# Optimization experiments

Measured on AMD Instinct MI355X. Metric: run time of the kernel, lower is better.

Reference implementation:

```python
import jax, jax.numpy as jnp
import numpy as np

N_TIME, N_BATCH, N_STATE, N_FORCE = 64, 8192, 32, 16
DT = 0.05          # implicit (backward-Euler) step size
NEWTON_ITERS = 6   # fixed Newton-Raphson iteration count (converges well below fp32 eps here)


def setup_inputs() -> dict:
    key = jax.random.key(0)
    k = jax.random.split(key, 5)
    return {
        "y0": jax.random.normal(k[0], (N_BATCH, N_STATE), jnp.float32) * 0.1,
        "forces": jax.random.normal(k[1], (N_TIME, N_BATCH, N_FORCE), jnp.float32),
        "W": jax.random.normal(k[2], (N_STATE, N_STATE), jnp.float32) / np.float32(np.sqrt(N_STATE)),
        "U": jax.random.normal(k[3], (N_STATE, N_FORCE), jnp.float32) / np.float32(np.sqrt(N_FORCE)),
        "b": jax.random.normal(k[4], (N_STATE,), jnp.float32) * 0.01,
        "n": N_TIME,
    }


def reference(y0, forces, W, U, b, n):
    """Sequential recursive nonlinear solve, block_size=1, ZeroPredictor guess.

    Each step solves R(y_k) = y_k - y_{k-1} - dt*tanh(W y_k + U u_k + b) = 0
    via Newton-Raphson with a batched dense solve of the diagonal Jacobian
    block J[1] = I - dt*diag(1-t^2) W (the Thomas factorization for a single
    step reduces to this dense solve).
    """
    S = y0.shape[-1]
    I = jnp.eye(S, dtype=y0.dtype)

    def step(y_prev, u):
        fu = u @ U.T + b                      # [B,S] constant per Newton solve
        y = jnp.zeros_like(y_prev)            # ZeroPredictor initial guess
        for _ in range(NEWTON_ITERS):         # plain Newton-Raphson
            t = jnp.tanh(y @ W.T + fu)        # [B,S]
            R = y - y_prev - DT * t           # residual [B,S]
            J = I - DT * ((1.0 - t * t)[..., :, None] * W)  # [B,S,S] dR/dy
            y = y - jnp.linalg.solve(J, R[..., None])[..., 0]
        return y, y

    _, ys = jax.lax.scan(step, y0, forces[1:n])   # sequential recursion over time
    return jnp.concatenate([y0[None], ys], axis=0)  # result[0] = y0
```

## Files before the change

kernel.cpp:

```cpp
#include <hip/hip_runtime.h>

#define NT 64
#define NB 8192
#define NS 32
#define NF 16
#define DT 0.05f
#define FP_ITERS 4
#define YSTR 36
#define USTR 20

typedef float f32x2 __attribute__((ext_vector_type(2)));
typedef float f32x4 __attribute__((ext_vector_type(4)));

__device__ __forceinline__ float tanh_fast(float x) {
    float e = __expf(2.0f * x);
    float r = __builtin_amdgcn_rcpf(e + 1.0f);
    return fmaf(-2.0f, r, 1.0f);
}

__global__ __launch_bounds__(256) void rnes_kernel(
    const float* __restrict__ y0,
    const float* __restrict__ forces,
    const float* __restrict__ W,
    const float* __restrict__ U,
    const float* __restrict__ bias,
    float* __restrict__ out)
{
    const int lane = threadIdx.x & 63;
    const int wv   = threadIdx.x >> 6;
    const int b    = lane >> 4;
    const int p    = lane & 15;
    const int batch = blockIdx.x * 16 + wv * 4 + b;

    __shared__ __align__(16) float Ysh[4][4 * YSTR];
    __shared__ __align__(16) float Ush[4][4 * USTR];
    float* Yw = Ysh[wv] + b * YSTR;
    float* Uw = Ush[wv] + b * USTR;

    f32x2 W2[NS];
#pragma unroll
    for (int k = 0; k < NS; k += 4) {
        f32x4 r0 = *(const f32x4*)(W + (2*p)   * NS + k);
        f32x4 r1 = *(const f32x4*)(W + (2*p+1) * NS + k);
#pragma unroll
        for (int e = 0; e < 4; ++e) W2[k+e] = (f32x2){r0[e], r1[e]};
    }
    f32x2 U2[NF];
#pragma unroll
    for (int f = 0; f < NF; f += 4) {
        f32x4 r0 = *(const f32x4*)(U + (2*p)   * NF + f);
        f32x4 r1 = *(const f32x4*)(U + (2*p+1) * NF + f);
#pragma unroll
        for (int e = 0; e < 4; ++e) U2[f+e] = (f32x2){r0[e], r1[e]};
    }
    const f32x2 b2 = *(const f32x2*)(bias + 2*p);

    f32x2 yp = *(const f32x2*)(y0 + (size_t)batch * NS + 2*p);
    *(f32x2*)(out + (size_t)batch * NS + 2*p) = yp;
    *(f32x2*)(Yw + 2*p) = yp;
    asm volatile("" ::: "memory");

    float fpre = forces[((size_t)1 * NB + batch) * NF + p];

    for (int k = 1; k < NT; ++k) {
        Uw[p] = fpre;
        asm volatile("" ::: "memory");

        f32x2 fu = b2;
#pragma unroll
        for (int f = 0; f < NF; f += 4) {
            f32x4 u4 = *(const f32x4*)(Uw + f);
            fu = U2[f+0] * u4[0] + fu;
            fu = U2[f+1] * u4[1] + fu;
            fu = U2[f+2] * u4[2] + fu;
            fu = U2[f+3] * u4[3] + fu;
        }

        {
            int kn = (k + 1 < NT) ? (k + 1) : (NT - 1);
            fpre = forces[((size_t)kn * NB + batch) * NF + p];
        }

        f32x2 y = yp;
#pragma unroll
        for (int it = 0; it < FP_ITERS; ++it) {
            f32x2 z = fu;
#pragma unroll
            for (int i = 0; i < NS; i += 4) {
                f32x4 yv = *(const f32x4*)(Yw + i);
                z = W2[i+0] * yv[0] + z;
                z = W2[i+1] * yv[1] + z;
                z = W2[i+2] * yv[2] + z;
                z = W2[i+3] * yv[3] + z;
            }
            float t0 = tanh_fast(z[0]);
            float t1 = tanh_fast(z[1]);
            y[0] = fmaf(DT, t0, yp[0]);
            y[1] = fmaf(DT, t1, yp[1]);
            asm volatile("" ::: "memory");
            *(f32x2*)(Yw + 2*p) = y;
            asm volatile("" ::: "memory");
        }

        yp = y;
        *(f32x2*)(out + ((size_t)k * NB + batch) * NS + 2*p) = yp;
    }
}

extern "C" void kernel_launch(void* const* d_in, const int* in_sizes, int n_in,
                              void* d_out, int out_size, void* d_ws, size_t ws_size,
                              hipStream_t stream) {
    const float* y0     = (const float*)d_in[0];
    const float* forces = (const float*)d_in[1];
    const float* W      = (const float*)d_in[2];
    const float* U      = (const float*)d_in[3];
    const float* b      = (const float*)d_in[4];
    float* out = (float*)d_out;

    dim3 grid(NB / 16);
    dim3 block(256);
    rnes_kernel<<<grid, block, 0, stream>>>(y0, forces, W, U, b, out);
}
```

Baseline: 172.2 us.

## Cut fixed-point iterations, load forces as vectors, split FMA accumulator chains

Lowers the fixed-point iteration count per time step from 4 to 3, which removes about a quarter of the inner matvec and tanh work on the serial critical path. It also drops the LDS staging of forces: each lane now loads the full 16-float force row directly into registers as four float4 loads. The matvec and force-projection accumulations are split into two independent chains to shorten FMA dependency latency. tanh now uses exp2 directly, and the launch bounds request two blocks per CU. The main risk is accuracy: one fewer contraction iteration leaves more residual error, and the per-lane vector force loads add register pressure and redundant global traffic.

```diff
diff --git a/kernel.cpp b/kernel.cpp
--- a/kernel.cpp
+++ b/kernel.cpp
@@ -5,20 +5,25 @@
 #define NS 32
 #define NF 16
 #define DT 0.05f
-#define FP_ITERS 4
+#define FP_ITERS 3
 #define YSTR 36
-#define USTR 20
 
 typedef float f32x2 __attribute__((ext_vector_type(2)));
 typedef float f32x4 __attribute__((ext_vector_type(4)));
 
-__device__ __forceinline__ float tanh_fast(float x) {
-    float e = __expf(2.0f * x);
-    float r = __builtin_amdgcn_rcpf(e + 1.0f);
-    return fmaf(-2.0f, r, 1.0f);
+__device__ __forceinline__ f32x2 tanh2(f32x2 x) {
+    const float K = 2.8853900817779268f;
+    float e0 = __builtin_amdgcn_exp2f(K * x[0]);
+    float e1 = __builtin_amdgcn_exp2f(K * x[1]);
+    float r0 = __builtin_amdgcn_rcpf(e0 + 1.0f);
+    float r1 = __builtin_amdgcn_rcpf(e1 + 1.0f);
+    f32x2 r;
+    r[0] = fmaf(-2.0f, r0, 1.0f);
+    r[1] = fmaf(-2.0f, r1, 1.0f);
+    return r;
 }
 
-__global__ __launch_bounds__(256) void rnes_kernel(
+__global__ __launch_bounds__(256, 2) void rnes_kernel(
     const float* __restrict__ y0,
     const float* __restrict__ forces,
     const float* __restrict__ W,
@@ -33,9 +38,7 @@
     const int batch = blockIdx.x * 16 + wv * 4 + b;
 
     __shared__ __align__(16) float Ysh[4][4 * YSTR];
-    __shared__ __align__(16) float Ush[4][4 * USTR];
     float* Yw = Ysh[wv] + b * YSTR;
-    float* Uw = Ush[wv] + b * USTR;
 
     f32x2 W2[NS];
 #pragma unroll
@@ -60,50 +63,52 @@
     *(f32x2*)(Yw + 2*p) = yp;
     asm volatile("" ::: "memory");
 
-    float fpre = forces[((size_t)1 * NB + batch) * NF + p];
+    const size_t fstep = (size_t)NB * NF;
+    const f32x4* fb = (const f32x4*)(forces + (size_t)batch * NF);
+    f32x4 upf[4];
+#pragma unroll
+    for (int j = 0; j < 4; ++j) upf[j] = fb[(fstep >> 2) + j];
 
     for (int k = 1; k < NT; ++k) {
-        Uw[p] = fpre;
-        asm volatile("" ::: "memory");
-
-        f32x2 fu = b2;
+        f32x2 a0 = b2, a1 = (f32x2){0.f, 0.f};
 #pragma unroll
         for (int f = 0; f < NF; f += 4) {
-            f32x4 u4 = *(const f32x4*)(Uw + f);
-            fu = U2[f+0] * u4[0] + fu;
-            fu = U2[f+1] * u4[1] + fu;
-            fu = U2[f+2] * u4[2] + fu;
-            fu = U2[f+3] * u4[3] + fu;
+            f32x4 u4 = upf[f >> 2];
+            a0 = U2[f+0] * u4[0] + a0;
+            a1 = U2[f+1] * u4[1] + a1;
+            a0 = U2[f+2] * u4[2] + a0;
+            a1 = U2[f+3] * u4[3] + a1;
         }
+        const f32x2 fu = a0 + a1;
 
         {
             int kn = (k + 1 < NT) ? (k + 1) : (NT - 1);
-            fpre = forces[((size_t)kn * NB + batch) * NF + p];
+#pragma unroll
+            for (int j = 0; j < 4; ++j) upf[j] = fb[(size_t)kn * (fstep >> 2) + j];
         }
 
         f32x2 y = yp;
 #pragma unroll
         for (int it = 0; it < FP_ITERS; ++it) {
-            f32x2 z = fu;
+            f32x2 z0 = fu, z1 = (f32x2){0.f, 0.f};
 #pragma unroll
-            for (int i = 0; i < NS; i += 4) {
-                f32x4 yv = *(const f32x4*)(Yw + i);
-                z = W2[i+0] * yv[0] + z;
-                z = W2[i+1] * yv[1] + z;
-                z = W2[i+2] * yv[2] + z;
-                z = W2[i+3] * yv[3] + z;
+            for (int i = 0; i < 8; ++i) {
+                f32x4 yv = ((const f32x4*)Yw)[i];
+                z0 = W2[4*i+0] * yv[0] + z0;
+                z1 = W2[4*i+1] * yv[1] + z1;
+                z0 = W2[4*i+2] * yv[2] + z0;
+                z1 = W2[4*i+3] * yv[3] + z1;
             }
-            float t0 = tanh_fast(z[0]);
-            float t1 = tanh_fast(z[1]);
-            y[0] = fmaf(DT, t0, yp[0]);
-            y[1] = fmaf(DT, t1, yp[1]);
+            f32x2 t = tanh2(z0 + z1);
+            y[0] = fmaf(DT, t[0], yp[0]);
+            y[1] = fmaf(DT, t[1], yp[1]);
             asm volatile("" ::: "memory");
             *(f32x2*)(Yw + 2*p) = y;
             asm volatile("" ::: "memory");
         }
 
         yp = y;
-        *(f32x2*)(out + ((size_t)k * NB + batch) * NS + 2*p) = yp;
+        *(f32x2*)(out + ((size_t)k * NB + batch) * NS + 2*p) = y;
     }
 }
 
```

New measurement: 160.4 us. 1.07x faster.
